# Kernel optimization log

Hardware: AMD Instinct MI355X
Metric: run time of the kernel (lower is better)

Reference implementation:

```python
import jax, jax.numpy as jnp
import numpy as np

NUM_NODES = 50000
NUM_EDGES = 1600000
NUM_GRAPHS = 64
K_HOPS = 3


def setup_inputs() -> dict:
    key = jax.random.key(0)
    ks = jax.random.split(key, 8)
    d_in, d_h, d_out = 128, 512, 16
    x = jax.random.normal(ks[0], (NUM_NODES, d_in), dtype=jnp.float32)
    edge_index = jax.random.randint(ks[1], (2, NUM_EDGES), 0, NUM_NODES, dtype=jnp.int64)
    batch = jnp.sort(jax.random.randint(ks[2], (NUM_NODES,), 0, NUM_GRAPHS, dtype=jnp.int64))
    w1 = jax.random.normal(ks[3], (d_in, d_h), dtype=jnp.float32) / np.sqrt(d_in)
    b1 = jnp.zeros((d_h,), dtype=jnp.float32)
    w2 = jax.random.normal(ks[4], (d_h, d_h), dtype=jnp.float32) / np.sqrt(d_h)
    b2 = jnp.zeros((d_h,), dtype=jnp.float32)
    wc = jax.random.normal(ks[5], (d_h, d_out), dtype=jnp.float32) / np.sqrt(d_h)
    bc = jnp.zeros((d_out,), dtype=jnp.float32)
    return {"x": x, "edge_index": edge_index, "batch": batch,
            "w1": w1, "b1": b1, "w2": w2, "b2": b2, "wc": wc, "bc": bc}


def _propagate(x, row, col, norm):
    # one hop: out[r] += x[c] * norm  (degree-normalized scatter-add)
    msg = x[col] * norm[:, None]                      # [E+N, d]
    return jax.ops.segment_sum(msg, row, num_segments=NUM_NODES)


def reference(x, edge_index, batch, w1, b1, w2, b2, wc, bc):
    # add self loops
    loops = jnp.arange(NUM_NODES, dtype=edge_index.dtype)
    row = jnp.concatenate([edge_index[0], loops])
    col = jnp.concatenate([edge_index[1], loops])
    deg = jax.ops.segment_sum(jnp.ones_like(row, dtype=jnp.float32), row,
                              num_segments=NUM_NODES)
    deg = jnp.clip(deg, 1.0)
    norm = 1.0 / deg[row]                             # [E+N]
    # K-hop propagation (eval mode: dropout / drop_node inactive)
    h = x
    for _ in range(K_HOPS):
        h = _propagate(h, row, col, norm)
    # MLP
    h = jax.nn.relu(h @ w1 + b1)
    h = h @ w2 + b2
    # global mean pool over graphs
    sums = jax.ops.segment_sum(h, batch, num_segments=NUM_GRAPHS)
    cnts = jax.ops.segment_sum(jnp.ones((h.shape[0],), dtype=h.dtype), batch,
                               num_segments=NUM_GRAPHS)
    pooled = sums / jnp.clip(cnts, 1.0)[:, None]      # [G, d_h]
    return pooled @ wc + bc                            # [G, out]
```

## Files before the change

kernel.cpp:

```cpp
#include <hip/hip_runtime.h>
#include <hip/hip_bf16.h>
#include <hip/hip_fp8.h>

#define N_NODES 50000
#define N_EDGES 1600000
#define N_GRAPHS 64
#define D_IN 128
#define D_H 512
#define D_OUT 16

#define NBUK 391
#define BUK_CAP 4608
#define P1_EDGES 4096
#define P1_BLOCKS ((N_EDGES + P1_EDGES - 1) / P1_EDGES)

#define MSPLIT 8

typedef short bf16x8 __attribute__((ext_vector_type(8)));
typedef float f32x4 __attribute__((ext_vector_type(4)));
typedef float f32x2 __attribute__((ext_vector_type(2)));

static __device__ __forceinline__ unsigned short f2bf(float f) {
    __hip_bfloat16 h = __float2bfloat16(f);
    return *(unsigned short*)&h;
}

static __device__ __forceinline__ float2 fp8x2_dec(unsigned short u) {
    __hip_fp8x2_e4m3 p;
    p.__x = (__hip_fp8x2_storage_t)u;
    return static_cast<float2>(p);
}

static __device__ __forceinline__ unsigned short fp8x2_enc(float a, float b) {
    __hip_fp8_e4m3 pa(a), pb(b);
    return (unsigned short)((unsigned)pa.__x | ((unsigned)pb.__x << 8));
}

static __device__ __forceinline__ void dec16_add(uint4 u, f32x2* acc) {
    unsigned vv[4] = {u.x, u.y, u.z, u.w};
#pragma unroll
    for (int w = 0; w < 4; ++w) {
        float2 a = fp8x2_dec((unsigned short)(vv[w] & 0xFFFFu));
        float2 b = fp8x2_dec((unsigned short)(vv[w] >> 16));
        f32x2 av; av.x = a.x; av.y = a.y;
        f32x2 bv; bv.x = b.x; bv.y = b.y;
        acc[w * 2 + 0] += av;
        acc[w * 2 + 1] += bv;
    }
}


__global__ __launch_bounds__(512) void partition_edges(const int* __restrict__ row,
                                                       const int* __restrict__ col,
                                                       int* __restrict__ bucket_cnt,
                                                       unsigned* __restrict__ edge_buf) {
    __shared__ unsigned recs[P1_EDGES];
    __shared__ unsigned sorted[P1_EDGES];
    __shared__ int hist4[4][NBUK];
    __shared__ int cur4[4][NBUK];
    __shared__ int gbase[NBUK];
    __shared__ int scan[512];
    int tid = threadIdx.x;
    int w2 = tid >> 7;
    int e0 = blockIdx.x * P1_EDGES;
    int m = N_EDGES - e0; if (m > P1_EDGES) m = P1_EDGES;

    for (int i = tid; i < 4 * NBUK; i += 512) ((int*)hist4)[i] = 0;
    for (int i = tid; i < 4 * NBUK; i += 512) ((int*)cur4)[i] = 0;
    __syncthreads();
    for (int i = tid; i < m; i += 512) {
        int r = row[e0 + i];
        int c = col[e0 + i];
        int buk = r >> 7;
        recs[i] = ((unsigned)buk << 23) | ((unsigned)(r & 127) << 16) | (unsigned)c;
        atomicAdd(&hist4[w2][buk], 1);
    }
    __syncthreads();
    int tot = 0;
    if (tid < NBUK) tot = hist4[0][tid] + hist4[1][tid] + hist4[2][tid] + hist4[3][tid];
    scan[tid] = (tid < NBUK) ? tot : 0;
    __syncthreads();
    for (int off = 1; off < 512; off <<= 1) {
        int v = (tid >= off) ? scan[tid - off] : 0;
        __syncthreads();
        scan[tid] += v;
        __syncthreads();
    }
    if (tid < NBUK) {
        int run = (tid == 0) ? 0 : scan[tid - 1];
        gbase[tid] = (tot > 0) ? atomicAdd(&bucket_cnt[tid], tot) : 0;
#pragma unroll
        for (int w = 0; w < 4; ++w) {
            int c = hist4[w][tid];
            hist4[w][tid] = run;
            run += c;
        }
    }
    __syncthreads();
    for (int i = tid; i < m; i += 512) {
        unsigned rec = recs[i];
        int buk = rec >> 23;
        int rank = atomicAdd(&cur4[w2][buk], 1);
        sorted[hist4[w2][buk] + rank] = rec;
    }
    __syncthreads();
    for (int p = tid; p < m; p += 512) {
        unsigned rec = sorted[p];
        int buk = rec >> 23;
        edge_buf[(size_t)buk * BUK_CAP + gbase[buk] + (p - hist4[0][buk])] = rec;
    }
}

__global__ __launch_bounds__(512) void finalize_csr(const unsigned* __restrict__ edge_buf,
                                                    const int* __restrict__ bucket_cnt,
                                                    int* __restrict__ rowptr,
                                                    float* __restrict__ invdeg,
                                                    unsigned short* __restrict__ csr_col) {
    __shared__ int hist[128], excl[128], cur[128];
    __shared__ int scan[512];
    int b = blockIdx.x;
    int tid = threadIdx.x;
    scan[tid] = (tid < NBUK) ? bucket_cnt[tid] : 0;
    __syncthreads();
    for (int off = 1; off < 512; off <<= 1) {
        int v = (tid >= off) ? scan[tid - off] : 0;
        __syncthreads();
        scan[tid] += v;
        __syncthreads();
    }
    int cnt = bucket_cnt[b];
    int base = (b == 0) ? 0 : scan[b - 1];
    const unsigned* src = edge_buf + (size_t)b * BUK_CAP;
    __syncthreads();
    if (tid < 128) { hist[tid] = 0; cur[tid] = 0; }
    __syncthreads();
    for (int i = tid; i < cnt; i += 512)
        atomicAdd(&hist[(src[i] >> 16) & 127], 1);
    __syncthreads();
    scan[tid] = (tid < 128) ? hist[tid] : 0;
    __syncthreads();
    for (int off = 1; off < 512; off <<= 1) {
        int v = (tid >= off) ? scan[tid - off] : 0;
        __syncthreads();
        scan[tid] += v;
        __syncthreads();
    }
    if (tid < 128) excl[tid] = (tid == 0) ? 0 : scan[tid - 1];
    __syncthreads();
    int r = b * 128 + tid;
    if (tid < 128 && r < N_NODES) {
        rowptr[r] = base + excl[tid];
        invdeg[r] = 1.0f / (float)(hist[tid] + 1);
    }
    if (b == NBUK - 1 && tid == 0) rowptr[N_NODES] = base + cnt;
    for (int i = tid; i < cnt; i += 512) {
        unsigned rec = src[i];
        int rl = (rec >> 16) & 127;
        int pos = excl[rl] + atomicAdd(&cur[rl], 1);
        csr_col[base + pos] = (unsigned short)(rec & 0xFFFFu);
    }
}


__global__ __launch_bounds__(256) void prep(const float* __restrict__ x,
                                            unsigned short* __restrict__ xf,
                                            const float* __restrict__ w1,
                                            unsigned short* __restrict__ w1p,
                                            const float* __restrict__ w2,
                                            const float* __restrict__ wc,
                                            const float* __restrict__ b2,
                                            const float* __restrict__ bc,
                                            const int* __restrict__ batch,
                                            float* __restrict__ wcomb,
                                            float* __restrict__ bcomb,
                                            int* __restrict__ gcnt,
                                            int* __restrict__ gstart,
                                            unsigned short* __restrict__ h0f,
                                            unsigned short* __restrict__ h1f) {
    int b = blockIdx.x;
    int tid = threadIdx.x;
    if (b < 12500) {
        int i = b * 256 + tid;
        float2 v = ((const float2*)x)[i];
        xf[i] = fp8x2_enc(v.x, v.y);
        return;
    }
    if (b < 12756) {
        int i = (b - 12500) * 256 + tid;
        int j = i & 7, lane = (i >> 3) & 63, s = (i >> 9) & 3, t = i >> 11;
        int k = s * 32 + (lane >> 4) * 8 + j;
        int n = t * 16 + (lane & 15);
        w1p[i] = f2bf(w1[(size_t)k * D_H + n]);
        return;
    }
    int fb = b - 12756;
    if (fb == 33) {
        if (tid < N_GRAPHS) {
            int g = tid;
            int lo = 0, hi = N_NODES;
            while (lo < hi) { int mid = (lo + hi) >> 1; if (batch[mid] < g) lo = mid + 1; else hi = mid; }
            int a = lo;
            lo = 0; hi = N_NODES;
            while (lo < hi) { int mid = (lo + hi) >> 1; if (batch[mid] < g + 1) lo = mid + 1; else hi = mid; }
            gcnt[g] = lo - a;
            gstart[g] = a;
            if (g == N_GRAPHS - 1) gstart[N_GRAPHS] = N_NODES;
        } else if (tid >= 64 && tid < 256) {
            int t = tid - 64;
            unsigned short* bp = (t < 64) ? xf : (t < 128 ? h0f : h1f);
            bp[(size_t)N_NODES * 64 + (t & 63)] = 0;
        }
        return;
    }
    int o = tid & 15, kl = tid >> 4;
    int k = fb * 16 + kl;
    if (k > D_H) return;
    const float* wr = (k < D_H) ? (w2 + (size_t)k * D_H) : b2;
    float s = 0.f;
    for (int j = 0; j < D_H; j += 4) {
        s += wr[j + 0] * wc[(j + 0) * D_OUT + o]
           + wr[j + 1] * wc[(j + 1) * D_OUT + o]
           + wr[j + 2] * wc[(j + 2) * D_OUT + o]
           + wr[j + 3] * wc[(j + 3) * D_OUT + o];
    }
    if (k < D_H) wcomb[k * D_OUT + o] = s;
    else         bcomb[o] = s + bc[o];
}


__global__ __launch_bounds__(256) void propagate_fp8(const unsigned short* __restrict__ xin,
                                                     unsigned short* __restrict__ out8,
                                                     unsigned* __restrict__ out16,
                                                     int last, float extra,
                                                     const int* __restrict__ rowptr,
                                                     const unsigned short* __restrict__ csr_col,
                                                     const float* __restrict__ invdeg) {
    int lane = threadIdx.x & 63;
    int wave = threadIdx.x >> 6;
    int l8   = lane & 7;
    int grp  = lane >> 3;
    int r = blockIdx.x * 32 + wave * 8 + grp;
    bool rv = (r < N_NODES);
    int rc = rv ? r : 0;
    int beg = rowptr[rc], end = rowptr[rc + 1];
    int nn = rv ? (end - beg) : 0;

    int nmax = nn;
    { int t = __shfl_xor(nmax, 8, 64);  if (t > nmax) nmax = t; }
    { int t = __shfl_xor(nmax, 16, 64); if (t > nmax) nmax = t; }
    { int t = __shfl_xor(nmax, 32, 64); if (t > nmax) nmax = t; }

    f32x2 acc[8];
#pragma unroll
    for (int i = 0; i < 8; ++i) acc[i] = (f32x2){0.f, 0.f};
    {
        uint4 u = *(const uint4*)(xin + (size_t)rc * 64 + l8 * 8);
        dec16_add(u, acc);
    }

    int base = lane & 56;
    auto ldidx = [&](int jb) -> int {
        int jj = jb + l8;
        int idx = (jj < nn) ? beg + jj : 0;
        unsigned short cl = csr_col[idx];
        return (jj < nn) ? (int)cl : N_NODES;
    };

    int nb = (nmax + 7) >> 3;
    if (nb > 0) {
        uint4 uA[8], uB[8];
        {
            int cv = ldidx(0);
#pragma unroll
            for (int q = 0; q < 8; ++q) {
                int c = __shfl(cv, base + q, 64);
                uA[q] = *(const uint4*)(xin + (size_t)c * 64 + l8 * 8);
            }
        }
        int cvn = ldidx(8);
        int k = 0;
        while (true) {
            if (k + 1 < nb) {
#pragma unroll
                for (int q = 0; q < 8; ++q) {
                    int c = __shfl(cvn, base + q, 64);
                    uB[q] = *(const uint4*)(xin + (size_t)c * 64 + l8 * 8);
                }
            }
            cvn = ldidx((k + 2) * 8);
#pragma unroll
            for (int q = 0; q < 8; ++q) dec16_add(uA[q], acc);
            ++k;
            if (k >= nb) break;
            if (k + 1 < nb) {
#pragma unroll
                for (int q = 0; q < 8; ++q) {
                    int c = __shfl(cvn, base + q, 64);
                    uA[q] = *(const uint4*)(xin + (size_t)c * 64 + l8 * 8);
                }
            }
            cvn = ldidx((k + 2) * 8);
#pragma unroll
            for (int q = 0; q < 8; ++q) dec16_add(uB[q], acc);
            ++k;
            if (k >= nb) break;
        }
    }

    if (!rv) return;

    float s = invdeg[r] * extra;
#pragma unroll
    for (int i = 0; i < 8; ++i) acc[i] *= s;

    if (last) {
        uint4 w0, w1v;
        w0.x = (unsigned)f2bf(acc[0].x) | ((unsigned)f2bf(acc[0].y) << 16);
        w0.y = (unsigned)f2bf(acc[1].x) | ((unsigned)f2bf(acc[1].y) << 16);
        w0.z = (unsigned)f2bf(acc[2].x) | ((unsigned)f2bf(acc[2].y) << 16);
        w0.w = (unsigned)f2bf(acc[3].x) | ((unsigned)f2bf(acc[3].y) << 16);
        w1v.x = (unsigned)f2bf(acc[4].x) | ((unsigned)f2bf(acc[4].y) << 16);
        w1v.y = (unsigned)f2bf(acc[5].x) | ((unsigned)f2bf(acc[5].y) << 16);
        w1v.z = (unsigned)f2bf(acc[6].x) | ((unsigned)f2bf(acc[6].y) << 16);
        w1v.w = (unsigned)f2bf(acc[7].x) | ((unsigned)f2bf(acc[7].y) << 16);
        unsigned* dst = out16 + (size_t)r * 64 + l8 * 8;
        *(uint4*)dst = w0;
        *(uint4*)(dst + 4) = w1v;
    } else {
        uint4 w;
        w.x = (unsigned)fp8x2_enc(acc[0].x, acc[0].y) | ((unsigned)fp8x2_enc(acc[1].x, acc[1].y) << 16);
        w.y = (unsigned)fp8x2_enc(acc[2].x, acc[2].y) | ((unsigned)fp8x2_enc(acc[3].x, acc[3].y) << 16);
        w.z = (unsigned)fp8x2_enc(acc[4].x, acc[4].y) | ((unsigned)fp8x2_enc(acc[5].x, acc[5].y) << 16);
        w.w = (unsigned)fp8x2_enc(acc[6].x, acc[6].y) | ((unsigned)fp8x2_enc(acc[7].x, acc[7].y) << 16);
        *(uint4*)(out8 + (size_t)r * 64 + l8 * 8) = w;
    }
}


__global__ __launch_bounds__(256) void gemm_graph_pool(const unsigned short* __restrict__ h3b,
                                                       const unsigned short* __restrict__ w1p,
                                                       const float* __restrict__ b1,
                                                       const int* __restrict__ gstart,
                                                       float* __restrict__ gsum) {
    __shared__ float wsum[4][128];
    int tid = threadIdx.x;
    int lane = tid & 63, wave = tid >> 6;
    int quad = lane >> 4, l15 = lane & 15;
    int g = blockIdx.x;
    int nbase = blockIdx.y * 128;
    int ms = blockIdx.z;
    int r0 = gstart[g], r1 = gstart[g + 1];

    float b1v[8];
#pragma unroll
    for (int t = 0; t < 8; ++t) b1v[t] = b1[nbase + t * 16 + l15];

    const unsigned short* bbase = w1p + ((size_t)(blockIdx.y * 8) * 4 * 64 + lane) * 8;

    float gaccT[8];
#pragma unroll
    for (int t = 0; t < 8; ++t) gaccT[t] = 0.f;

    for (int mbase = r0 + ms * 64; mbase < r1; mbase += 64 * MSPLIT) {
        int m = mbase + wave * 16 + l15;
        int mc = m < N_NODES ? m : N_NODES - 1;
        const unsigned short* arow = h3b + (size_t)mc * 128 + quad * 8;
        bf16x8 afrag[4];
#pragma unroll
        for (int s = 0; s < 4; ++s)
            afrag[s] = *(const bf16x8*)(arow + s * 32);

        int rowbase = mbase + wave * 16 + quad * 4;
#pragma unroll
        for (int t = 0; t < 8; ++t) {
            f32x4 acc = (f32x4){0.f, 0.f, 0.f, 0.f};
#pragma unroll
            for (int s = 0; s < 4; ++s) {
                bf16x8 bfrag = *(const bf16x8*)(bbase + (size_t)(t * 4 + s) * 64 * 8);
                acc = __builtin_amdgcn_mfma_f32_16x16x32_bf16(afrag[s], bfrag, acc, 0, 0, 0);
            }
#pragma unroll
            for (int rg = 0; rg < 4; ++rg) {
                float v = acc[rg] + b1v[t];
                v = v > 0.f ? v : 0.f;
                gaccT[t] += (rowbase + rg < r1) ? v : 0.f;
            }
        }
    }
#pragma unroll
    for (int t = 0; t < 8; ++t) {
        gaccT[t] += __shfl_xor(gaccT[t], 16, 64);
        gaccT[t] += __shfl_xor(gaccT[t], 32, 64);
    }
    if (quad == 0) {
#pragma unroll
        for (int t = 0; t < 8; ++t)
            wsum[wave][t * 16 + l15] = gaccT[t];
    }
    __syncthreads();
    if (tid < 128)
        gsum[((size_t)ms * N_GRAPHS + g) * D_H + nbase + tid] =
            wsum[0][tid] + wsum[1][tid] + wsum[2][tid] + wsum[3][tid];
}


__global__ __launch_bounds__(256) void final_pool(const float* __restrict__ gsum,
                                                  const int* __restrict__ gcnt,
                                                  const float* __restrict__ wcomb,
                                                  const float* __restrict__ bcomb,
                                                  float* __restrict__ out) {
    int g = blockIdx.x;
    int tid = threadIdx.x;
    __shared__ float p[D_H];
    __shared__ float part[16][17];
    int c = gcnt[g]; if (c < 1) c = 1;
    float inv = 1.0f / (float)c;
#pragma unroll
    for (int h = 0; h < 2; ++h) {
        int i = tid + h * 256;
        float v = 0.f;
#pragma unroll
        for (int ms = 0; ms < MSPLIT; ++ms)
            v += gsum[((size_t)ms * N_GRAPHS + g) * D_H + i];
        p[i] = v * inv;
    }
    __syncthreads();
    int o = tid & 15, ch = tid >> 4;
    int k0 = ch * 32;
    float s = 0.f;
    for (int k = k0; k < k0 + 32; ++k)
        s += p[k] * wcomb[k * D_OUT + o];
    part[ch][o] = s;
    __syncthreads();
    if (tid < D_OUT) {
        float t = bcomb[tid];
        for (int ch2 = 0; ch2 < 16; ++ch2) t += part[ch2][tid];
        out[g * D_OUT + tid] = t;
    }
}


extern "C" void kernel_launch(void* const* d_in, const int* in_sizes, int n_in,
                              void* d_out, int out_size, void* d_ws, size_t ws_size,
                              hipStream_t stream) {
    const float* x     = (const float*)d_in[0];
    const int*   eidx  = (const int*)d_in[1];
    const int*   batch = (const int*)d_in[2];
    const float* w1    = (const float*)d_in[3];
    const float* b1    = (const float*)d_in[4];
    const float* w2    = (const float*)d_in[5];
    const float* b2    = (const float*)d_in[6];
    const float* wc    = (const float*)d_in[7];
    const float* bc    = (const float*)d_in[8];
    float* out = (float*)d_out;
    const int* row = eidx;
    const int* col = eidx + N_EDGES;

    char* p = (char*)d_ws;
    auto alloc = [&](size_t bytes) { char* q = p; p += (bytes + 255) & ~(size_t)255; return q; };
    char* zbase = p;
    int*   bucket_cnt = (int*)alloc((size_t)NBUK * 4);
    size_t zbytes = (size_t)(p - zbase);
    float* gsum    = (float*)alloc((size_t)MSPLIT * N_GRAPHS * D_H * 4);
    int*   rowptr  = (int*)alloc((size_t)(N_NODES + 1) * 4);
    int*   gcnt    = (int*)alloc((size_t)N_GRAPHS * 4);
    int*   gstart  = (int*)alloc((size_t)(N_GRAPHS + 1) * 4);
    float* invdeg  = (float*)alloc((size_t)N_NODES * 4);
    float* wcomb   = (float*)alloc((size_t)D_H * D_OUT * 4);
    float* bcomb   = (float*)alloc((size_t)D_OUT * 4);
    unsigned* edge_buf = (unsigned*)alloc((size_t)NBUK * BUK_CAP * 4);
    unsigned short* csr_col = (unsigned short*)alloc((size_t)N_EDGES * 2);
    unsigned short* xf  = (unsigned short*)alloc((size_t)(N_NODES + 1) * 64 * 2);
    unsigned short* h0f = (unsigned short*)alloc((size_t)(N_NODES + 1) * 64 * 2);
    unsigned short* h1f = (unsigned short*)alloc((size_t)(N_NODES + 1) * 64 * 2);
    unsigned* h3b  = (unsigned*)alloc((size_t)N_NODES * 64 * 4);
    unsigned short* w1p = (unsigned short*)alloc((size_t)D_IN * D_H * 2);

    (void)hipMemsetAsync(zbase, 0, zbytes, stream);

    prep<<<12790, 256, 0, stream>>>(x, xf, w1, w1p, w2, wc, b2, bc, batch,
                                    wcomb, bcomb, gcnt, gstart, h0f, h1f);

    partition_edges<<<P1_BLOCKS, 512, 0, stream>>>(row, col, bucket_cnt, edge_buf);
    finalize_csr<<<NBUK, 512, 0, stream>>>(edge_buf, bucket_cnt, rowptr, invdeg, csr_col);

    int pgrid = (N_NODES + 31) / 32;
    propagate_fp8<<<pgrid, 256, 0, stream>>>(xf,  h0f, nullptr, 0, 8.0f,
                                             rowptr, csr_col, invdeg);
    propagate_fp8<<<pgrid, 256, 0, stream>>>(h0f, h1f, nullptr, 0, 8.0f,
                                             rowptr, csr_col, invdeg);
    propagate_fp8<<<pgrid, 256, 0, stream>>>(h1f, nullptr, h3b, 1, 1.0f / 64.0f,
                                             rowptr, csr_col, invdeg);

    dim3 ggrid(N_GRAPHS, D_H / 128, MSPLIT);
    gemm_graph_pool<<<ggrid, 256, 0, stream>>>((const unsigned short*)h3b, w1p, b1,
                                               gstart, gsum);
    final_pool<<<N_GRAPHS, 256, 0, stream>>>(gsum, gcnt, wcomb, bcomb, out);
}
```

Measured before the change: 235.4 us.

## Split fp8 feature propagation into two column halves for cache locality

Stores the fp8 node features as two separate 64-column halves and runs each hop as two launches, one per half. Each launch gathers only 64 bytes per neighbour, so the working set of each gather (about 3.2 MB) is halved and should sit better in the L2 or last-level cache. In exchange the CSR indices and rowptr are read twice, there are twice as many launches, each gather is a narrower uint2 load, and the double-buffered prefetch loop is replaced by a simpler single-buffer loop.

```diff
diff --git a/kernel.cpp b/kernel.cpp
--- a/kernel.cpp
+++ b/kernel.cpp
@@ -16,6 +16,8 @@
 
 #define MSPLIT 8
 
+#define HSTRIDE ((size_t)(N_NODES + 1) * 32)
+
 typedef short bf16x8 __attribute__((ext_vector_type(8)));
 typedef float f32x4 __attribute__((ext_vector_type(4)));
 typedef float f32x2 __attribute__((ext_vector_type(2)));
@@ -36,10 +38,10 @@
     return (unsigned short)((unsigned)pa.__x | ((unsigned)pb.__x << 8));
 }
 
-static __device__ __forceinline__ void dec16_add(uint4 u, f32x2* acc) {
-    unsigned vv[4] = {u.x, u.y, u.z, u.w};
-#pragma unroll
-    for (int w = 0; w < 4; ++w) {
+static __device__ __forceinline__ void dec8_add(uint2 u, f32x2* acc) {
+    unsigned vv[2] = {u.x, u.y};
+#pragma unroll
+    for (int w = 0; w < 2; ++w) {
         float2 a = fp8x2_dec((unsigned short)(vv[w] & 0xFFFFu));
         float2 b = fp8x2_dec((unsigned short)(vv[w] >> 16));
         f32x2 av; av.x = a.x; av.y = a.y;
@@ -182,7 +184,9 @@
     if (b < 12500) {
         int i = b * 256 + tid;
         float2 v = ((const float2*)x)[i];
-        xf[i] = fp8x2_enc(v.x, v.y);
+        int n = i >> 6, j = i & 63;
+        int h = j >> 5, s = j & 31;
+        xf[(size_t)h * HSTRIDE + (size_t)n * 32 + s] = fp8x2_enc(v.x, v.y);
         return;
     }
     if (b < 12756) {
@@ -207,8 +211,11 @@
             if (g == N_GRAPHS - 1) gstart[N_GRAPHS] = N_NODES;
         } else if (tid >= 64 && tid < 256) {
             int t = tid - 64;
-            unsigned short* bp = (t < 64) ? xf : (t < 128 ? h0f : h1f);
-            bp[(size_t)N_NODES * 64 + (t & 63)] = 0;
+            if (t < 192) {
+                int which = t >> 5;
+                unsigned short* bp = (which < 2) ? xf : (which < 4 ? h0f : h1f);
+                bp[(size_t)(which & 1) * HSTRIDE + (size_t)N_NODES * 32 + (t & 31)] = 0;
+            }
         }
         return;
     }
@@ -228,13 +235,13 @@
 }
 
 
-__global__ __launch_bounds__(256) void propagate_fp8(const unsigned short* __restrict__ xin,
-                                                     unsigned short* __restrict__ out8,
-                                                     unsigned* __restrict__ out16,
-                                                     int last, float extra,
-                                                     const int* __restrict__ rowptr,
-                                                     const unsigned short* __restrict__ csr_col,
-                                                     const float* __restrict__ invdeg) {
+__global__ __launch_bounds__(256) void propagate_half(const unsigned short* __restrict__ xin,
+                                                      unsigned short* __restrict__ out8,
+                                                      unsigned* __restrict__ out16,
+                                                      int last, float extra,
+                                                      const int* __restrict__ rowptr,
+                                                      const unsigned short* __restrict__ csr_col,
+                                                      const float* __restrict__ invdeg) {
     int lane = threadIdx.x & 63;
     int wave = threadIdx.x >> 6;
     int l8   = lane & 7;
@@ -250,12 +257,12 @@
     { int t = __shfl_xor(nmax, 16, 64); if (t > nmax) nmax = t; }
     { int t = __shfl_xor(nmax, 32, 64); if (t > nmax) nmax = t; }
 
-    f32x2 acc[8];
-#pragma unroll
-    for (int i = 0; i < 8; ++i) acc[i] = (f32x2){0.f, 0.f};
+    f32x2 acc[4];
+#pragma unroll
+    for (int i = 0; i < 4; ++i) acc[i] = (f32x2){0.f, 0.f};
     {
-        uint4 u = *(const uint4*)(xin + (size_t)rc * 64 + l8 * 8);
-        dec16_add(u, acc);
+        uint2 u = *(const uint2*)(xin + (size_t)rc * 32 + l8 * 4);
+        dec8_add(u, acc);
     }
 
     int base = lane & 56;
@@ -266,73 +273,38 @@
         return (jj < nn) ? (int)cl : N_NODES;
     };
 
-    int nb = (nmax + 7) >> 3;
-    if (nb > 0) {
-        uint4 uA[8], uB[8];
-        {
-            int cv = ldidx(0);
-#pragma unroll
-            for (int q = 0; q < 8; ++q) {
-                int c = __shfl(cv, base + q, 64);
-                uA[q] = *(const uint4*)(xin + (size_t)c * 64 + l8 * 8);
-            }
+    int cv = ldidx(0);
+    for (int jb = 0; jb < nmax; jb += 8) {
+        uint2 u[8];
+#pragma unroll
+        for (int q = 0; q < 8; ++q) {
+            int c = __shfl(cv, base + q, 64);
+            u[q] = *(const uint2*)(xin + (size_t)c * 32 + l8 * 4);
         }
-        int cvn = ldidx(8);
-        int k = 0;
-        while (true) {
-            if (k + 1 < nb) {
-#pragma unroll
-                for (int q = 0; q < 8; ++q) {
-                    int c = __shfl(cvn, base + q, 64);
-                    uB[q] = *(const uint4*)(xin + (size_t)c * 64 + l8 * 8);
-                }
-            }
-            cvn = ldidx((k + 2) * 8);
-#pragma unroll
-            for (int q = 0; q < 8; ++q) dec16_add(uA[q], acc);
-            ++k;
-            if (k >= nb) break;
-            if (k + 1 < nb) {
-#pragma unroll
-                for (int q = 0; q < 8; ++q) {
-                    int c = __shfl(cvn, base + q, 64);
-                    uA[q] = *(const uint4*)(xin + (size_t)c * 64 + l8 * 8);
-                }
-            }
-            cvn = ldidx((k + 2) * 8);
-#pragma unroll
-            for (int q = 0; q < 8; ++q) dec16_add(uB[q], acc);
-            ++k;
-            if (k >= nb) break;
-        }
+        int cvn = ldidx(jb + 8);
+#pragma unroll
+        for (int q = 0; q < 8; ++q) dec8_add(u[q], acc);
+        cv = cvn;
     }
 
     if (!rv) return;
 
     float s = invdeg[r] * extra;
 #pragma unroll
-    for (int i = 0; i < 8; ++i) acc[i] *= s;
+    for (int i = 0; i < 4; ++i) acc[i] *= s;
 
     if (last) {
-        uint4 w0, w1v;
-        w0.x = (unsigned)f2bf(acc[0].x) | ((unsigned)f2bf(acc[0].y) << 16);
-        w0.y = (unsigned)f2bf(acc[1].x) | ((unsigned)f2bf(acc[1].y) << 16);
-        w0.z = (unsigned)f2bf(acc[2].x) | ((unsigned)f2bf(acc[2].y) << 16);
-        w0.w = (unsigned)f2bf(acc[3].x) | ((unsigned)f2bf(acc[3].y) << 16);
-        w1v.x = (unsigned)f2bf(acc[4].x) | ((unsigned)f2bf(acc[4].y) << 16);
-        w1v.y = (unsigned)f2bf(acc[5].x) | ((unsigned)f2bf(acc[5].y) << 16);
-        w1v.z = (unsigned)f2bf(acc[6].x) | ((unsigned)f2bf(acc[6].y) << 16);
-        w1v.w = (unsigned)f2bf(acc[7].x) | ((unsigned)f2bf(acc[7].y) << 16);
-        unsigned* dst = out16 + (size_t)r * 64 + l8 * 8;
-        *(uint4*)dst = w0;
-        *(uint4*)(dst + 4) = w1v;
+        uint4 w;
+        w.x = (unsigned)f2bf(acc[0].x) | ((unsigned)f2bf(acc[0].y) << 16);
+        w.y = (unsigned)f2bf(acc[1].x) | ((unsigned)f2bf(acc[1].y) << 16);
+        w.z = (unsigned)f2bf(acc[2].x) | ((unsigned)f2bf(acc[2].y) << 16);
+        w.w = (unsigned)f2bf(acc[3].x) | ((unsigned)f2bf(acc[3].y) << 16);
+        *(uint4*)(out16 + (size_t)r * 64 + l8 * 4) = w;
     } else {
-        uint4 w;
+        uint2 w;
         w.x = (unsigned)fp8x2_enc(acc[0].x, acc[0].y) | ((unsigned)fp8x2_enc(acc[1].x, acc[1].y) << 16);
         w.y = (unsigned)fp8x2_enc(acc[2].x, acc[2].y) | ((unsigned)fp8x2_enc(acc[3].x, acc[3].y) << 16);
-        w.z = (unsigned)fp8x2_enc(acc[4].x, acc[4].y) | ((unsigned)fp8x2_enc(acc[5].x, acc[5].y) << 16);
-        w.w = (unsigned)fp8x2_enc(acc[6].x, acc[6].y) | ((unsigned)fp8x2_enc(acc[7].x, acc[7].y) << 16);
-        *(uint4*)(out8 + (size_t)r * 64 + l8 * 8) = w;
+        *(uint2*)(out8 + (size_t)r * 32 + l8 * 4) = w;
     }
 }
 
@@ -470,9 +442,9 @@
     float* bcomb   = (float*)alloc((size_t)D_OUT * 4);
     unsigned* edge_buf = (unsigned*)alloc((size_t)NBUK * BUK_CAP * 4);
     unsigned short* csr_col = (unsigned short*)alloc((size_t)N_EDGES * 2);
-    unsigned short* xf  = (unsigned short*)alloc((size_t)(N_NODES + 1) * 64 * 2);
-    unsigned short* h0f = (unsigned short*)alloc((size_t)(N_NODES + 1) * 64 * 2);
-    unsigned short* h1f = (unsigned short*)alloc((size_t)(N_NODES + 1) * 64 * 2);
+    unsigned short* xf  = (unsigned short*)alloc(HSTRIDE * 2 * 2);
+    unsigned short* h0f = (unsigned short*)alloc(HSTRIDE * 2 * 2);
+    unsigned short* h1f = (unsigned short*)alloc(HSTRIDE * 2 * 2);
     unsigned* h3b  = (unsigned*)alloc((size_t)N_NODES * 64 * 4);
     unsigned short* w1p = (unsigned short*)alloc((size_t)D_IN * D_H * 2);
 
@@ -485,12 +457,18 @@
     finalize_csr<<<NBUK, 512, 0, stream>>>(edge_buf, bucket_cnt, rowptr, invdeg, csr_col);
 
     int pgrid = (N_NODES + 31) / 32;
-    propagate_fp8<<<pgrid, 256, 0, stream>>>(xf,  h0f, nullptr, 0, 8.0f,
-                                             rowptr, csr_col, invdeg);
-    propagate_fp8<<<pgrid, 256, 0, stream>>>(h0f, h1f, nullptr, 0, 8.0f,
-                                             rowptr, csr_col, invdeg);
-    propagate_fp8<<<pgrid, 256, 0, stream>>>(h1f, nullptr, h3b, 1, 1.0f / 64.0f,
-                                             rowptr, csr_col, invdeg);
+    propagate_half<<<pgrid, 256, 0, stream>>>(xf,           h0f,           nullptr, 0, 8.0f,
+                                              rowptr, csr_col, invdeg);
+    propagate_half<<<pgrid, 256, 0, stream>>>(xf + HSTRIDE, h0f + HSTRIDE, nullptr, 0, 8.0f,
+                                              rowptr, csr_col, invdeg);
+    propagate_half<<<pgrid, 256, 0, stream>>>(h0f,           h1f,           nullptr, 0, 8.0f,
+                                              rowptr, csr_col, invdeg);
+    propagate_half<<<pgrid, 256, 0, stream>>>(h0f + HSTRIDE, h1f + HSTRIDE, nullptr, 0, 8.0f,
+                                              rowptr, csr_col, invdeg);
+    propagate_half<<<pgrid, 256, 0, stream>>>(h1f,           nullptr, h3b,      1, 1.0f / 64.0f,
+                                              rowptr, csr_col, invdeg);
+    propagate_half<<<pgrid, 256, 0, stream>>>(h1f + HSTRIDE, nullptr, h3b + 32, 1, 1.0f / 64.0f,
+                                              rowptr, csr_col, invdeg);
 
     dim3 ggrid(N_GRAPHS, D_H / 128, MSPLIT);
     gemm_graph_pool<<<ggrid, 256, 0, stream>>>((const unsigned short*)h3b, w1p, b1,
```

Measured after the change: 253.3 us. +7.6%, slower.
